# Kernel optimization log

Measured on AMD Instinct MI355X. Metric: run time of the kernel, lower is better.

## Reference

```python
import jax, jax.numpy as jnp
import numpy as np

# Static conv hyperparameters (match init_kwargs / setup_inputs)
PAD = 1
DIL = 1
STRIDE_VAL = 2.5          # continuous stride value used in setup_inputs
INT_STRIDE = 2            # floor(STRIDE_VAL): used for output-size arithmetic (static)


def _bilinear_take(x, pos, axis):
    """Linearly interpolate x along `axis` at fractional positions `pos`.

    pos has shape [O, K]; the sampled axis of x is replaced by the two axes
    (O, K). Out-of-range samples contribute zero (deform-conv convention).
    """
    n = x.shape[axis]
    p0 = jnp.floor(pos).astype(jnp.int32)
    frac = (pos - p0.astype(pos.dtype))
    out_shape = x.shape[:axis] + pos.shape + x.shape[axis + 1:]
    bshape = (1,) * axis + pos.shape + (1,) * (x.ndim - axis - 1)

    def take(p):
        valid = ((p >= 0) & (p < n)).astype(x.dtype).reshape(bshape)
        v = jnp.take(x, jnp.clip(p, 0, n - 1).reshape(-1), axis=axis)
        return v.reshape(out_shape) * valid

    w = frac.reshape(bshape).astype(x.dtype)
    return take(p0) * (1.0 - w) + take(p0 + 1) * w


def setup_inputs() -> dict:
    key = jax.random.key(0)
    k1, k2, k3 = jax.random.split(key, 3)
    x = jax.random.normal(k1, (32, 128, 64, 64), dtype=jnp.float32)
    weight = jax.random.normal(k2, (256, 128, 3, 3), dtype=jnp.float32) * 0.05
    bias = jax.random.normal(k3, (256,), dtype=jnp.float32)
    stride_h = jnp.full((1,), STRIDE_VAL, dtype=jnp.float32)
    stride_w = jnp.full((1,), STRIDE_VAL, dtype=jnp.float32)
    return {"x": x, "weight": weight, "bias": bias,
            "stride_h": stride_h, "stride_w": stride_w}


def reference(x, weight, bias, stride_h, stride_w):
    B, C, H, W = x.shape
    O, _, KH, KW = weight.shape
    # output size uses floor(stride), exactly as StrideConv2dFunction._output_size
    OH = (H + 2 * PAD - DIL * (KH - 1) - 1) // INT_STRIDE + 1
    OW = (W + 2 * PAD - DIL * (KW - 1) - 1) // INT_STRIDE + 1
    # fractional im2col sampling positions: out_idx * stride - pad + k * dilation
    pos_h = (jnp.arange(OH, dtype=jnp.float32)[:, None] * stride_h[0]
             - PAD + jnp.arange(KH, dtype=jnp.float32)[None, :] * DIL)  # [OH,KH]
    pos_w = (jnp.arange(OW, dtype=jnp.float32)[:, None] * stride_w[0]
             - PAD + jnp.arange(KW, dtype=jnp.float32)[None, :] * DIL)  # [OW,KW]
    rows = _bilinear_take(x, pos_h, axis=2)          # [B,C,OH,KH,W]
    patches = _bilinear_take(rows, pos_w, axis=4)    # [B,C,OH,KH,OW,KW]
    out = jnp.einsum('bcpkql,ockl->bopq', patches, weight)  # [B,O,OH,OW]
    return out + bias[None, :, None, None]
```

## Files before the change

### kernel.cpp

```cpp
#include <hip/hip_runtime.h>
#include <cstddef>

#define BB  32
#define CC  128
#define HH  64
#define WW  64
#define OO  256
#define OHH 32
#define OWW 32
#define YSTR 196
#define PSTR 296
#define ROWE (32 * YSTR)

typedef __bf16 bf16x8 __attribute__((ext_vector_type(8)));
typedef __bf16 bf16x4 __attribute__((ext_vector_type(4)));
typedef float  f32x4  __attribute__((ext_vector_type(4)));

__global__ void wtrans_bf16_kernel(const float* __restrict__ w, __bf16* __restrict__ wt) {
    int idx = blockIdx.x * 256 + threadIdx.x;
    if (idx >= OO * 9 * CC) return;
    int c    = idx & 127;
    int rest = idx >> 7;
    int k    = rest % 9;
    int o    = rest / 9;
    wt[idx] = (__bf16)w[((size_t)o * CC + c) * 9 + k];
}

__global__ __launch_bounds__(512, 2)
void conv_mfma_kernel(const float* __restrict__ x, const __bf16* __restrict__ wt,
                      const float* __restrict__ bias, const float* __restrict__ shp,
                      const float* __restrict__ swp, float* __restrict__ out) {
    __shared__ __align__(16) __bf16 yrbuf[4 + 4 * ROWE];
    __shared__ __align__(16) __bf16 pT[128 * PSTR];

    const int tid = threadIdx.x;
    const int b   = blockIdx.x;
    const int p0  = blockIdx.y * 4;
    const float sh = shp[0];
    const float sw = swp[0];

    float fh_[4];
    int   hb_[4];
    bool  oob[4];
#pragma unroll
    for (int pi = 0; pi < 4; ++pi) {
        float hpos = (float)(p0 + pi) * sh - 1.0f;
        float hbf  = floorf(hpos);
        fh_[pi] = hpos - hbf;
        hb_[pi] = (int)hbf;
        oob[pi] = (hb_[pi] >= HH || hb_[pi] <= -4);
    }

    if (oob[0] && oob[1] && oob[2] && oob[3]) {
#pragma unroll
        for (int j = 0; j < 16; ++j) {
            int fi = j * 512 + tid;
            int o  = fi >> 5;
            int rem = fi & 31;
            int pi = rem >> 3;
            int qf = rem & 7;
            float bv = bias[o];
            float4 r; r.x = bv; r.y = bv; r.z = bv; r.w = bv;
            *(float4*)(out + (((size_t)b * OO + o) * OHH + p0 + pi) * OWW + qf * 4) = r;
        }
        return;
    }

    const int piA = tid >> 7;
    const int t7  = tid & 127;
    const int cA  = t7 >> 2;
    const int cg0 = (t7 & 3) * 16;
    const float fhA = fh_[piA];
    int  hrA[4];
    bool rvA[4];
#pragma unroll
    for (int r = 0; r < 4; ++r) {
        hrA[r] = hb_[piA] + r;
        rvA[r] = (hrA[r] >= 0) && (hrA[r] < HH);
    }
    __bf16* yrA = yrbuf + 4 + piA * ROWE;

    const int piB = tid >> 7;
    const int qB  = (tid >> 2) & 31;
    const int cB  = (tid & 3) * 8;
    const float wposB = (float)qB * sw - 1.0f;
    const float wbfB  = floorf(wposB);
    const float fw    = wposB - wbfB;
    const int   wbq   = (int)wbfB;
    const int   wba   = min(wbq & ~3, 60);
    const int   e     = wbq - wba;
    const bool  g1 = e >= 1, g2 = e >= 2, g3 = e >= 3;
    bool mv[4];
#pragma unroll
    for (int j = 0; j < 4; ++j) mv[j] = ((unsigned)(wbq + j) < (unsigned)WW);
    const bool qDead = (wbq >= WW);
    const __bf16* yrB = yrbuf + 4 + piB * ROWE;
    __bf16* pqRow = pT + (piB * 32 + qB) * PSTR;

    const int wv = tid >> 6;
    const int l  = tid & 63;
    const int lr = l & 15;
    const int lg = l >> 4;
    const int o0 = wv * 32;

    f32x4 acc[2][8];
#pragma unroll
    for (int ot = 0; ot < 2; ++ot)
#pragma unroll
        for (int nt = 0; nt < 8; ++nt) acc[ot][nt] = (f32x4)0.0f;

    if (tid < 4) yrbuf[tid] = (__bf16)0.0f;

    if (qDead) {
        bf16x4 z;
        z[0] = (__bf16)0.0f; z[1] = (__bf16)0.0f; z[2] = (__bf16)0.0f; z[3] = (__bf16)0.0f;
#pragma unroll
        for (int kk = 0; kk < 9; ++kk) {
            *(bf16x4*)(pqRow + kk * 32 + cB)     = z;
            *(bf16x4*)(pqRow + kk * 32 + cB + 4) = z;
        }
    }

    for (int chunk = 0; chunk < 4; ++chunk) {
        const int c0 = chunk * 32;

        {
            const float* xp = x + ((size_t)(b * CC + c0 + cA) * HH) * WW;
            float4 v[4][4];
#pragma unroll
            for (int r = 0; r < 4; ++r) {
                if (rvA[r]) {
                    const float* rp = xp + (size_t)hrA[r] * WW + cg0;
#pragma unroll
                    for (int g = 0; g < 4; ++g) v[r][g] = *(const float4*)(rp + g * 4);
                } else {
#pragma unroll
                    for (int g = 0; g < 4; ++g) { v[r][g].x = 0.f; v[r][g].y = 0.f; v[r][g].z = 0.f; v[r][g].w = 0.f; }
                }
            }
            __bf16* yw = yrA + cA * YSTR + cg0;
#pragma unroll
            for (int kh = 0; kh < 3; ++kh) {
#pragma unroll
                for (int g = 0; g < 4; ++g) {
                    bf16x4 t;
                    t[0] = (__bf16)(v[kh][g].x + fhA * (v[kh + 1][g].x - v[kh][g].x));
                    t[1] = (__bf16)(v[kh][g].y + fhA * (v[kh + 1][g].y - v[kh][g].y));
                    t[2] = (__bf16)(v[kh][g].z + fhA * (v[kh + 1][g].z - v[kh][g].z));
                    t[3] = (__bf16)(v[kh][g].w + fhA * (v[kh + 1][g].w - v[kh][g].w));
                    *(bf16x4*)(yw + kh * 64 + g * 4) = t;
                }
            }
        }
        __syncthreads();

        if (!qDead) {
#pragma unroll
            for (int g = 0; g < 2; ++g) {
                const int cc0 = cB + g * 4;
                bf16x4 rlo[12], rhi[12];
#pragma unroll
                for (int ci = 0; ci < 4; ++ci)
#pragma unroll
                    for (int kh = 0; kh < 3; ++kh) {
                        const __bf16* yc = yrB + (cc0 + ci) * YSTR + kh * 64 + wba;
                        rlo[ci * 3 + kh] = *(const bf16x4*)yc;
                        rhi[ci * 3 + kh] = *(const bf16x4*)(yc + 4);
                    }
                float tv[3][3][4];
#pragma unroll
                for (int ci = 0; ci < 4; ++ci)
#pragma unroll
                    for (int kh = 0; kh < 3; ++kh) {
                        bf16x4 a  = rlo[ci * 3 + kh];
                        bf16x4 bq = rhi[ci * 3 + kh];
                        float v0 = (float)a[0], v1 = (float)a[1], v2 = (float)a[2], v3 = (float)a[3];
                        float v4 = (float)bq[0], v5 = (float)bq[1], v6 = (float)bq[2];
                        float s0 = g1 ? v1 : v0; s0 = g2 ? v2 : s0; s0 = g3 ? v3 : s0;
                        float s1 = g1 ? v2 : v1; s1 = g2 ? v3 : s1; s1 = g3 ? v4 : s1;
                        float s2 = g1 ? v3 : v2; s2 = g2 ? v4 : s2; s2 = g3 ? v5 : s2;
                        float s3 = g1 ? v4 : v3; s3 = g2 ? v5 : s3; s3 = g3 ? v6 : s3;
                        s0 = mv[0] ? s0 : 0.0f;
                        s1 = mv[1] ? s1 : 0.0f;
                        s2 = mv[2] ? s2 : 0.0f;
                        s3 = mv[3] ? s3 : 0.0f;
                        tv[kh][0][ci] = s0 + fw * (s1 - s0);
                        tv[kh][1][ci] = s1 + fw * (s2 - s1);
                        tv[kh][2][ci] = s2 + fw * (s3 - s2);
                    }
#pragma unroll
                for (int kh = 0; kh < 3; ++kh)
#pragma unroll
                    for (int kw = 0; kw < 3; ++kw) {
                        bf16x4 pr;
                        pr[0] = (__bf16)tv[kh][kw][0];
                        pr[1] = (__bf16)tv[kh][kw][1];
                        pr[2] = (__bf16)tv[kh][kw][2];
                        pr[3] = (__bf16)tv[kh][kw][3];
                        *(bf16x4*)(pqRow + (kh * 3 + kw) * 32 + cc0) = pr;
                    }
            }
        }
        __syncthreads();

        __builtin_amdgcn_s_setprio(1);
#pragma unroll
        for (int k = 0; k < 9; ++k) {
            const __bf16* wp = wt + ((size_t)(o0 + lr) * 9 + k) * CC + c0 + lg * 8;
            bf16x8 a0 = *(const bf16x8*)(wp);
            bf16x8 a1 = *(const bf16x8*)(wp + (size_t)16 * 9 * CC);
            bf16x8 bfr[8];
#pragma unroll
            for (int nt = 0; nt < 8; ++nt)
                bfr[nt] = *(const bf16x8*)&pT[(nt * 16 + lr) * PSTR + k * 32 + lg * 8];
#pragma unroll
            for (int nt = 0; nt < 8; ++nt) {
                acc[0][nt] = __builtin_amdgcn_mfma_f32_16x16x32_bf16(a0, bfr[nt], acc[0][nt], 0, 0, 0);
                acc[1][nt] = __builtin_amdgcn_mfma_f32_16x16x32_bf16(a1, bfr[nt], acc[1][nt], 0, 0, 0);
            }
        }
        __builtin_amdgcn_s_setprio(0);
    }

#pragma unroll
    for (int ot = 0; ot < 2; ++ot) {
#pragma unroll
        for (int r = 0; r < 4; ++r) {
            int o = o0 + ot * 16 + lg * 4 + r;
            float bv = bias[o];
#pragma unroll
            for (int nt = 0; nt < 8; ++nt) {
                int pi = nt >> 1;
                int qc = (nt & 1) * 16 + lr;
                out[(((size_t)b * OO + o) * OHH + p0 + pi) * OWW + qc] = acc[ot][nt][r] + bv;
            }
        }
    }
}

__global__ __launch_bounds__(256)
void conv_fallback_kernel(const float* __restrict__ x, const float* __restrict__ w,
                          const float* __restrict__ bias, const float* __restrict__ shp,
                          const float* __restrict__ swp, float* __restrict__ out) {
    __shared__ __align__(16) float xr[4][WW];
    __shared__ __align__(16) float patch[9][OWW];
    const int tid = threadIdx.x;
    const int p = blockIdx.y;
    const int b = blockIdx.x;
    const float sh = shp[0];
    const float sw = swp[0];
    const float hpos = (float)p * sh - 1.0f;
    const float hbf  = floorf(hpos);
    const float fh   = hpos - hbf;
    const int   hb   = (int)hbf;
    const int og = tid & 63;
    const int qg = tid >> 6;
    const int o0 = og * 4;
    const int q0 = qg * 8;
    const int rr   = tid >> 6;
    const int colc = tid & 63;
    const int rowg = hb + rr;
    const bool rv = (rowg >= 0) && (rowg < HH);
    float acc[4][8];
#pragma unroll
    for (int i = 0; i < 4; ++i)
#pragma unroll
        for (int j = 0; j < 8; ++j) acc[i][j] = 0.0f;
    for (int c = 0; c < CC; ++c) {
        float vv = 0.0f;
        if (rv) vv = x[(((size_t)b * CC + c) * HH + rowg) * WW + colc];
        xr[rr][colc] = vv;
        __syncthreads();
        for (int it = tid; it < 9 * OWW; it += 256) {
            int k = it >> 5; int q = it & 31;
            int kh = k / 3;  int kw = k - kh * 3;
            float wpos = (float)q * sw - 1.0f + (float)kw;
            float wbf = floorf(wpos);
            float fwl = wpos - wbf;
            int wb = (int)wbf;
            float x00 = 0, x01 = 0, x10 = 0, x11 = 0;
            if (wb >= 0 && wb < WW)         { x00 = xr[kh][wb];     x10 = xr[kh + 1][wb]; }
            if (wb + 1 >= 0 && wb + 1 < WW) { x01 = xr[kh][wb + 1]; x11 = xr[kh + 1][wb + 1]; }
            float top = x00 * (1.0f - fwl) + x01 * fwl;
            float bot = x10 * (1.0f - fwl) + x11 * fwl;
            patch[k][q] = top * (1.0f - fh) + bot * fh;
        }
        __syncthreads();
        const float4* pv = (const float4*)&patch[0][0];
#pragma unroll
        for (int k = 0; k < 9; ++k) {
            const float* wb_ = w + (size_t)o0 * (CC * 9) + c * 9 + k;
            float wvv[4] = {wb_[0], wb_[1 * CC * 9], wb_[2 * CC * 9], wb_[3 * CC * 9]};
            float4 pa = pv[k * 8 + (q0 >> 2)];
            float4 pb = pv[k * 8 + (q0 >> 2) + 1];
#pragma unroll
            for (int oo2 = 0; oo2 < 4; ++oo2) {
                acc[oo2][0] += wvv[oo2] * pa.x; acc[oo2][1] += wvv[oo2] * pa.y;
                acc[oo2][2] += wvv[oo2] * pa.z; acc[oo2][3] += wvv[oo2] * pa.w;
                acc[oo2][4] += wvv[oo2] * pb.x; acc[oo2][5] += wvv[oo2] * pb.y;
                acc[oo2][6] += wvv[oo2] * pb.z; acc[oo2][7] += wvv[oo2] * pb.w;
            }
        }
    }
    float4 bv = ((const float4*)bias)[og];
    float bvv[4] = {bv.x, bv.y, bv.z, bv.w};
#pragma unroll
    for (int oo2 = 0; oo2 < 4; ++oo2) {
        size_t off = (((size_t)b * OO + o0 + oo2) * OHH + p) * OWW + q0;
        float4 r0, r1;
        r0.x = acc[oo2][0] + bvv[oo2]; r0.y = acc[oo2][1] + bvv[oo2];
        r0.z = acc[oo2][2] + bvv[oo2]; r0.w = acc[oo2][3] + bvv[oo2];
        r1.x = acc[oo2][4] + bvv[oo2]; r1.y = acc[oo2][5] + bvv[oo2];
        r1.z = acc[oo2][6] + bvv[oo2]; r1.w = acc[oo2][7] + bvv[oo2];
        *(float4*)(out + off)     = r0;
        *(float4*)(out + off + 4) = r1;
    }
}

extern "C" void kernel_launch(void* const* d_in, const int* in_sizes, int n_in,
                              void* d_out, int out_size, void* d_ws, size_t ws_size,
                              hipStream_t stream) {
    const float* x    = (const float*)d_in[0];
    const float* w    = (const float*)d_in[1];
    const float* bias = (const float*)d_in[2];
    const float* shp  = (const float*)d_in[3];
    const float* swp  = (const float*)d_in[4];
    float* out = (float*)d_out;

    const size_t wt_bytes = (size_t)OO * 9 * CC * sizeof(__bf16);
    if (ws_size >= wt_bytes) {
        __bf16* wtp = (__bf16*)d_ws;
        int n = OO * 9 * CC;
        wtrans_bf16_kernel<<<(n + 255) / 256, 256, 0, stream>>>(w, wtp);
        dim3 grid(BB, OHH / 4);
        conv_mfma_kernel<<<grid, 512, 0, stream>>>(x, wtp, bias, shp, swp, out);
    } else {
        dim3 grid(BB, OHH);
        conv_fallback_kernel<<<grid, 256, 0, stream>>>(x, w, bias, shp, swp, out);
    }
}
```

Baseline: 55.30 us.

## Warp-specialize conv into producer/consumer waves with double-buffered patch tiles

Splits the block into four producer waves and four MFMA consumer waves. The producers do the bilinear row and column interpolation into double-buffered LDS patch slots, and the consumers run the GEMM. They synchronise through workgroup-scope atomic counters with spin-waits instead of block-wide __syncthreads, so patch building for the next channel chunk can overlap the MFMA work on the current one. Each block now covers 2 output rows instead of 4, which doubles the grid and halves LDS use. The cost is that only half the waves issue MFMAs, weight loads are duplicated across twice as many blocks, and spin-wait polling adds overhead.

```diff
diff --git a/kernel.cpp b/kernel.cpp
--- a/kernel.cpp
+++ b/kernel.cpp
@@ -9,8 +9,9 @@
 #define OHH 32
 #define OWW 32
 #define YSTR 196
+#define ROWE (32 * YSTR)
 #define PSTR 296
-#define ROWE (32 * YSTR)
+#define PTSLOT (64 * PSTR)
 
 typedef __bf16 bf16x8 __attribute__((ext_vector_type(8)));
 typedef __bf16 bf16x4 __attribute__((ext_vector_type(4)));
@@ -30,33 +31,34 @@
 void conv_mfma_kernel(const float* __restrict__ x, const __bf16* __restrict__ wt,
                       const float* __restrict__ bias, const float* __restrict__ shp,
                       const float* __restrict__ swp, float* __restrict__ out) {
-    __shared__ __align__(16) __bf16 yrbuf[4 + 4 * ROWE];
-    __shared__ __align__(16) __bf16 pT[128 * PSTR];
+    __shared__ __align__(16) __bf16 yrbuf[4 + 2 * ROWE];
+    __shared__ __align__(16) __bf16 pT[2 * PTSLOT];
+    __shared__ int ydone, pdone, cdone;
 
     const int tid = threadIdx.x;
     const int b   = blockIdx.x;
-    const int p0  = blockIdx.y * 4;
+    const int p0  = blockIdx.y * 2;
     const float sh = shp[0];
     const float sw = swp[0];
 
-    float fh_[4];
-    int   hb_[4];
-    bool  oob[4];
-#pragma unroll
-    for (int pi = 0; pi < 4; ++pi) {
+    float fh_[2];
+    int   hb_[2];
+#pragma unroll
+    for (int pi = 0; pi < 2; ++pi) {
         float hpos = (float)(p0 + pi) * sh - 1.0f;
         float hbf  = floorf(hpos);
         fh_[pi] = hpos - hbf;
         hb_[pi] = (int)hbf;
-        oob[pi] = (hb_[pi] >= HH || hb_[pi] <= -4);
-    }
-
-    if (oob[0] && oob[1] && oob[2] && oob[3]) {
-#pragma unroll
-        for (int j = 0; j < 16; ++j) {
+    }
+    const bool oob0 = (hb_[0] >= HH || hb_[0] <= -4);
+    const bool oob1 = (hb_[1] >= HH || hb_[1] <= -4);
+
+    if (oob0 && oob1) {
+#pragma unroll
+        for (int j = 0; j < 8; ++j) {
             int fi = j * 512 + tid;
-            int o  = fi >> 5;
-            int rem = fi & 31;
+            int o  = fi >> 4;
+            int rem = fi & 15;
             int pi = rem >> 3;
             int qf = rem & 7;
             float bv = bias[o];
@@ -66,173 +68,218 @@
         return;
     }
 
-    const int piA = tid >> 7;
-    const int t7  = tid & 127;
-    const int cA  = t7 >> 2;
-    const int cg0 = (t7 & 3) * 16;
-    const float fhA = fh_[piA];
-    int  hrA[4];
-    bool rvA[4];
-#pragma unroll
-    for (int r = 0; r < 4; ++r) {
-        hrA[r] = hb_[piA] + r;
-        rvA[r] = (hrA[r] >= 0) && (hrA[r] < HH);
-    }
-    __bf16* yrA = yrbuf + 4 + piA * ROWE;
-
-    const int piB = tid >> 7;
-    const int qB  = (tid >> 2) & 31;
-    const int cB  = (tid & 3) * 8;
-    const float wposB = (float)qB * sw - 1.0f;
-    const float wbfB  = floorf(wposB);
-    const float fw    = wposB - wbfB;
-    const int   wbq   = (int)wbfB;
-    const int   wba   = min(wbq & ~3, 60);
-    const int   e     = wbq - wba;
-    const bool  g1 = e >= 1, g2 = e >= 2, g3 = e >= 3;
-    bool mv[4];
-#pragma unroll
-    for (int j = 0; j < 4; ++j) mv[j] = ((unsigned)(wbq + j) < (unsigned)WW);
-    const bool qDead = (wbq >= WW);
-    const __bf16* yrB = yrbuf + 4 + piB * ROWE;
-    __bf16* pqRow = pT + (piB * 32 + qB) * PSTR;
+    if (tid == 0) { ydone = 0; pdone = 0; cdone = 0; }
+    if (tid < 4) yrbuf[tid] = (__bf16)0.0f;
+    __syncthreads();
 
     const int wv = tid >> 6;
     const int l  = tid & 63;
     const int lr = l & 15;
     const int lg = l >> 4;
-    const int o0 = wv * 32;
-
-    f32x4 acc[2][8];
-#pragma unroll
-    for (int ot = 0; ot < 2; ++ot)
-#pragma unroll
-        for (int nt = 0; nt < 8; ++nt) acc[ot][nt] = (f32x4)0.0f;
-
-    if (tid < 4) yrbuf[tid] = (__bf16)0.0f;
-
-    if (qDead) {
-        bf16x4 z;
-        z[0] = (__bf16)0.0f; z[1] = (__bf16)0.0f; z[2] = (__bf16)0.0f; z[3] = (__bf16)0.0f;
-#pragma unroll
-        for (int kk = 0; kk < 9; ++kk) {
-            *(bf16x4*)(pqRow + kk * 32 + cB)     = z;
-            *(bf16x4*)(pqRow + kk * 32 + cB + 4) = z;
-        }
-    }
-
-    for (int chunk = 0; chunk < 4; ++chunk) {
-        const int c0 = chunk * 32;
-
-        {
-            const float* xp = x + ((size_t)(b * CC + c0 + cA) * HH) * WW;
-            float4 v[4][4];
-#pragma unroll
-            for (int r = 0; r < 4; ++r) {
-                if (rvA[r]) {
-                    const float* rp = xp + (size_t)hrA[r] * WW + cg0;
-#pragma unroll
-                    for (int g = 0; g < 4; ++g) v[r][g] = *(const float4*)(rp + g * 4);
-                } else {
-#pragma unroll
-                    for (int g = 0; g < 4; ++g) { v[r][g].x = 0.f; v[r][g].y = 0.f; v[r][g].z = 0.f; v[r][g].w = 0.f; }
+
+    auto waitge = [&](int* f, int t) {
+        while (__hip_atomic_load(f, __ATOMIC_RELAXED, __HIP_MEMORY_SCOPE_WORKGROUP) < t)
+            __builtin_amdgcn_s_sleep(2);
+        __threadfence_block();
+        __builtin_amdgcn_sched_barrier(0);
+    };
+    auto post = [&](int* f) {
+        __threadfence_block();
+        if ((tid & 63) == 0)
+            __hip_atomic_fetch_add(f, 1, __ATOMIC_RELAXED, __HIP_MEMORY_SCOPE_WORKGROUP);
+    };
+
+    if (wv < 4) {
+        const int piA = tid >> 7;
+        const int t7  = tid & 127;
+        const int cA  = t7 >> 2;
+        const int cg0 = (t7 & 3) * 16;
+        const float fhA = fh_[piA];
+        int  hrA[4];
+        bool rvA[4];
+#pragma unroll
+        for (int r = 0; r < 4; ++r) {
+            hrA[r] = hb_[piA] + r;
+            rvA[r] = (hrA[r] >= 0) && (hrA[r] < HH);
+        }
+        __bf16* yrA = yrbuf + 4 + piA * ROWE;
+
+        const int qB2  = tid >> 2;
+        const int pi2B = qB2 >> 5;
+        const int qB   = qB2 & 31;
+        const int cB   = (tid & 3) * 8;
+        const float wposB = (float)qB * sw - 1.0f;
+        const float wbfB  = floorf(wposB);
+        const float fw    = wposB - wbfB;
+        const int   wbq   = (int)wbfB;
+        const int   wba   = min(wbq & ~3, 60);
+        const int   e     = wbq - wba;
+        const bool  g1 = e >= 1, g2 = e >= 2, g3 = e >= 3;
+        bool mv[4];
+#pragma unroll
+        for (int j = 0; j < 4; ++j) mv[j] = ((unsigned)(wbq + j) < (unsigned)WW);
+        const bool qDead = (wbq >= WW);
+        const __bf16* yrB = yrbuf + 4 + pi2B * ROWE;
+
+        if (qDead) {
+            bf16x4 z;
+            z[0] = (__bf16)0.0f; z[1] = (__bf16)0.0f; z[2] = (__bf16)0.0f; z[3] = (__bf16)0.0f;
+#pragma unroll
+            for (int s = 0; s < 2; ++s) {
+                __bf16* pq = pT + s * PTSLOT + qB2 * PSTR;
+#pragma unroll
+                for (int kk = 0; kk < 9; ++kk) {
+                    *(bf16x4*)(pq + kk * 32 + cB)     = z;
+                    *(bf16x4*)(pq + kk * 32 + cB + 4) = z;
                 }
             }
-            __bf16* yw = yrA + cA * YSTR + cg0;
-#pragma unroll
-            for (int kh = 0; kh < 3; ++kh) {
-#pragma unroll
-                for (int g = 0; g < 4; ++g) {
-                    bf16x4 t;
-                    t[0] = (__bf16)(v[kh][g].x + fhA * (v[kh + 1][g].x - v[kh][g].x));
-                    t[1] = (__bf16)(v[kh][g].y + fhA * (v[kh + 1][g].y - v[kh][g].y));
-                    t[2] = (__bf16)(v[kh][g].z + fhA * (v[kh + 1][g].z - v[kh][g].z));
-                    t[3] = (__bf16)(v[kh][g].w + fhA * (v[kh + 1][g].w - v[kh][g].w));
-                    *(bf16x4*)(yw + kh * 64 + g * 4) = t;
+        }
+
+        for (int c = 0; c < 4; ++c) {
+            const int c0 = c * 32;
+            if (c >= 1) waitge(&pdone, 4 * c);
+
+            {
+                const float* xp = x + ((size_t)(b * CC + c0 + cA) * HH) * WW;
+                float4 v[4][4];
+#pragma unroll
+                for (int r = 0; r < 4; ++r) {
+                    if (rvA[r]) {
+                        const float* rp = xp + (size_t)hrA[r] * WW + cg0;
+#pragma unroll
+                        for (int g = 0; g < 4; ++g) v[r][g] = *(const float4*)(rp + g * 4);
+                    } else {
+#pragma unroll
+                        for (int g = 0; g < 4; ++g) { v[r][g].x = 0.f; v[r][g].y = 0.f; v[r][g].z = 0.f; v[r][g].w = 0.f; }
+                    }
                 }
-            }
-        }
-        __syncthreads();
-
-        if (!qDead) {
-#pragma unroll
-            for (int g = 0; g < 2; ++g) {
-                const int cc0 = cB + g * 4;
-                bf16x4 rlo[12], rhi[12];
-#pragma unroll
-                for (int ci = 0; ci < 4; ++ci)
-#pragma unroll
-                    for (int kh = 0; kh < 3; ++kh) {
-                        const __bf16* yc = yrB + (cc0 + ci) * YSTR + kh * 64 + wba;
-                        rlo[ci * 3 + kh] = *(const bf16x4*)yc;
-                        rhi[ci * 3 + kh] = *(const bf16x4*)(yc + 4);
+                __bf16* yw = yrA + cA * YSTR + cg0;
+#pragma unroll
+                for (int kh = 0; kh < 3; ++kh)
+#pragma unroll
+                    for (int g = 0; g < 4; ++g) {
+                        bf16x4 t;
+                        t[0] = (__bf16)(v[kh][g].x + fhA * (v[kh + 1][g].x - v[kh][g].x));
+                        t[1] = (__bf16)(v[kh][g].y + fhA * (v[kh + 1][g].y - v[kh][g].y));
+                        t[2] = (__bf16)(v[kh][g].z + fhA * (v[kh + 1][g].z - v[kh][g].z));
+                        t[3] = (__bf16)(v[kh][g].w + fhA * (v[kh + 1][g].w - v[kh][g].w));
+                        *(bf16x4*)(yw + kh * 64 + g * 4) = t;
                     }
-                float tv[3][3][4];
-#pragma unroll
-                for (int ci = 0; ci < 4; ++ci)
-#pragma unroll
-                    for (int kh = 0; kh < 3; ++kh) {
-                        bf16x4 a  = rlo[ci * 3 + kh];
-                        bf16x4 bq = rhi[ci * 3 + kh];
-                        float v0 = (float)a[0], v1 = (float)a[1], v2 = (float)a[2], v3 = (float)a[3];
-                        float v4 = (float)bq[0], v5 = (float)bq[1], v6 = (float)bq[2];
-                        float s0 = g1 ? v1 : v0; s0 = g2 ? v2 : s0; s0 = g3 ? v3 : s0;
-                        float s1 = g1 ? v2 : v1; s1 = g2 ? v3 : s1; s1 = g3 ? v4 : s1;
-                        float s2 = g1 ? v3 : v2; s2 = g2 ? v4 : s2; s2 = g3 ? v5 : s2;
-                        float s3 = g1 ? v4 : v3; s3 = g2 ? v5 : s3; s3 = g3 ? v6 : s3;
-                        s0 = mv[0] ? s0 : 0.0f;
-                        s1 = mv[1] ? s1 : 0.0f;
-                        s2 = mv[2] ? s2 : 0.0f;
-                        s3 = mv[3] ? s3 : 0.0f;
-                        tv[kh][0][ci] = s0 + fw * (s1 - s0);
-                        tv[kh][1][ci] = s1 + fw * (s2 - s1);
-                        tv[kh][2][ci] = s2 + fw * (s3 - s2);
-                    }
-#pragma unroll
-                for (int kh = 0; kh < 3; ++kh)
-#pragma unroll
-                    for (int kw = 0; kw < 3; ++kw) {
-                        bf16x4 pr;
-                        pr[0] = (__bf16)tv[kh][kw][0];
-                        pr[1] = (__bf16)tv[kh][kw][1];
-                        pr[2] = (__bf16)tv[kh][kw][2];
-                        pr[3] = (__bf16)tv[kh][kw][3];
-                        *(bf16x4*)(pqRow + (kh * 3 + kw) * 32 + cc0) = pr;
-                    }
-            }
-        }
-        __syncthreads();
-
+            }
+            post(&ydone);
+            waitge(&ydone, 4 * (c + 1));
+            if (c >= 2) waitge(&cdone, 4 * (c - 1));
+
+            if (!qDead) {
+                __bf16* pqRow = pT + (c & 1) * PTSLOT + qB2 * PSTR;
+#pragma unroll
+                for (int g = 0; g < 2; ++g) {
+                    const int cc0 = cB + g * 4;
+                    bf16x4 rlo[12], rhi[12];
+#pragma unroll
+                    for (int ci = 0; ci < 4; ++ci)
+#pragma unroll
+                        for (int kh = 0; kh < 3; ++kh) {
+                            const __bf16* yc = yrB + (cc0 + ci) * YSTR + kh * 64 + wba;
+                            rlo[ci * 3 + kh] = *(const bf16x4*)yc;
+                            rhi[ci * 3 + kh] = *(const bf16x4*)(yc + 4);
+                        }
+                    float tv[3][3][4];
+#pragma unroll
+                    for (int ci = 0; ci < 4; ++ci)
+#pragma unroll
+                        for (int kh = 0; kh < 3; ++kh) {
+                            bf16x4 a  = rlo[ci * 3 + kh];
+                            bf16x4 bq = rhi[ci * 3 + kh];
+                            float v0 = (float)a[0], v1 = (float)a[1], v2 = (float)a[2], v3 = (float)a[3];
+                            float v4 = (float)bq[0], v5 = (float)bq[1], v6 = (float)bq[2];
+                            float s0 = g1 ? v1 : v0; s0 = g2 ? v2 : s0; s0 = g3 ? v3 : s0;
+                            float s1 = g1 ? v2 : v1; s1 = g2 ? v3 : s1; s1 = g3 ? v4 : s1;
+                            float s2 = g1 ? v3 : v2; s2 = g2 ? v4 : s2; s2 = g3 ? v5 : s2;
+                            float s3 = g1 ? v4 : v3; s3 = g2 ? v5 : s3; s3 = g3 ? v6 : s3;
+                            s0 = mv[0] ? s0 : 0.0f;
+                            s1 = mv[1] ? s1 : 0.0f;
+                            s2 = mv[2] ? s2 : 0.0f;
+                            s3 = mv[3] ? s3 : 0.0f;
+                            tv[kh][0][ci] = s0 + fw * (s1 - s0);
+                            tv[kh][1][ci] = s1 + fw * (s2 - s1);
+                            tv[kh][2][ci] = s2 + fw * (s3 - s2);
+                        }
+#pragma unroll
+                    for (int kh = 0; kh < 3; ++kh)
+#pragma unroll
+                        for (int kw = 0; kw < 3; ++kw) {
+                            bf16x4 pr;
+                            pr[0] = (__bf16)tv[kh][kw][0];
+                            pr[1] = (__bf16)tv[kh][kw][1];
+                            pr[2] = (__bf16)tv[kh][kw][2];
+                            pr[3] = (__bf16)tv[kh][kw][3];
+                            *(bf16x4*)(pqRow + (kh * 3 + kw) * 32 + cc0) = pr;
+                        }
+                }
+            }
+            post(&pdone);
+        }
+        return;
+    }
+
+    const int o0 = (wv - 4) * 64;
+    f32x4 acc[4][4];
+#pragma unroll
+    for (int ot = 0; ot < 4; ++ot)
+#pragma unroll
+        for (int nt = 0; nt < 4; ++nt) acc[ot][nt] = (f32x4)0.0f;
+
+#pragma unroll
+    for (int c = 0; c < 4; ++c) {
+        const int c0 = c * 32;
+        waitge(&pdone, 4 * (c + 1));
+        const __bf16* pTs = pT + (c & 1) * PTSLOT;
         __builtin_amdgcn_s_setprio(1);
 #pragma unroll
         for (int k = 0; k < 9; ++k) {
             const __bf16* wp = wt + ((size_t)(o0 + lr) * 9 + k) * CC + c0 + lg * 8;
             bf16x8 a0 = *(const bf16x8*)(wp);
             bf16x8 a1 = *(const bf16x8*)(wp + (size_t)16 * 9 * CC);
-            bf16x8 bfr[8];
-#pragma unroll
-            for (int nt = 0; nt < 8; ++nt)
-                bfr[nt] = *(const bf16x8*)&pT[(nt * 16 + lr) * PSTR + k * 32 + lg * 8];
-#pragma unroll
-            for (int nt = 0; nt < 8; ++nt) {
-                acc[0][nt] = __builtin_amdgcn_mfma_f32_16x16x32_bf16(a0, bfr[nt], acc[0][nt], 0, 0, 0);
-                acc[1][nt] = __builtin_amdgcn_mfma_f32_16x16x32_bf16(a1, bfr[nt], acc[1][nt], 0, 0, 0);
-            }
+            bf16x8 a2 = *(const bf16x8*)(wp + (size_t)32 * 9 * CC);
+            bf16x8 a3 = *(const bf16x8*)(wp + (size_t)48 * 9 * CC);
+            bf16x8 b0 = *(const bf16x8*)&pTs[(0  + lr) * PSTR + k * 32 + lg * 8];
+            bf16x8 b1 = *(const bf16x8*)&pTs[(16 + lr) * PSTR + k * 32 + lg * 8];
+            bf16x8 b2 = *(const bf16x8*)&pTs[(32 + lr) * PSTR + k * 32 + lg * 8];
+            bf16x8 b3 = *(const bf16x8*)&pTs[(48 + lr) * PSTR + k * 32 + lg * 8];
+            acc[0][0] = __builtin_amdgcn_mfma_f32_16x16x32_bf16(a0, b0, acc[0][0], 0, 0, 0);
+            acc[0][1] = __builtin_amdgcn_mfma_f32_16x16x32_bf16(a0, b1, acc[0][1], 0, 0, 0);
+            acc[0][2] = __builtin_amdgcn_mfma_f32_16x16x32_bf16(a0, b2, acc[0][2], 0, 0, 0);
+            acc[0][3] = __builtin_amdgcn_mfma_f32_16x16x32_bf16(a0, b3, acc[0][3], 0, 0, 0);
+            acc[1][0] = __builtin_amdgcn_mfma_f32_16x16x32_bf16(a1, b0, acc[1][0], 0, 0, 0);
+            acc[1][1] = __builtin_amdgcn_mfma_f32_16x16x32_bf16(a1, b1, acc[1][1], 0, 0, 0);
+            acc[1][2] = __builtin_amdgcn_mfma_f32_16x16x32_bf16(a1, b2, acc[1][2], 0, 0, 0);
+            acc[1][3] = __builtin_amdgcn_mfma_f32_16x16x32_bf16(a1, b3, acc[1][3], 0, 0, 0);
+            acc[2][0] = __builtin_amdgcn_mfma_f32_16x16x32_bf16(a2, b0, acc[2][0], 0, 0, 0);
+            acc[2][1] = __builtin_amdgcn_mfma_f32_16x16x32_bf16(a2, b1, acc[2][1], 0, 0, 0);
+            acc[2][2] = __builtin_amdgcn_mfma_f32_16x16x32_bf16(a2, b2, acc[2][2], 0, 0, 0);
+            acc[2][3] = __builtin_amdgcn_mfma_f32_16x16x32_bf16(a2, b3, acc[2][3], 0, 0, 0);
+            acc[3][0] = __builtin_amdgcn_mfma_f32_16x16x32_bf16(a3, b0, acc[3][0], 0, 0, 0);
+            acc[3][1] = __builtin_amdgcn_mfma_f32_16x16x32_bf16(a3, b1, acc[3][1], 0, 0, 0);
+            acc[3][2] = __builtin_amdgcn_mfma_f32_16x16x32_bf16(a3, b2, acc[3][2], 0, 0, 0);
+            acc[3][3] = __builtin_amdgcn_mfma_f32_16x16x32_bf16(a3, b3, acc[3][3], 0, 0, 0);
         }
         __builtin_amdgcn_s_setprio(0);
-    }
-
-#pragma unroll
-    for (int ot = 0; ot < 2; ++ot) {
+        post(&cdone);
+    }
+
+#pragma unroll
+    for (int ot = 0; ot < 4; ++ot) {
 #pragma unroll
         for (int r = 0; r < 4; ++r) {
             int o = o0 + ot * 16 + lg * 4 + r;
             float bv = bias[o];
 #pragma unroll
-            for (int nt = 0; nt < 8; ++nt) {
-                int pi = nt >> 1;
-                int qc = (nt & 1) * 16 + lr;
-                out[(((size_t)b * OO + o) * OHH + p0 + pi) * OWW + qc] = acc[ot][nt][r] + bv;
+            for (int nt = 0; nt < 4; ++nt) {
+                int n  = nt * 16 + lr;
+                int pi = n >> 5;
+                int q  = n & 31;
+                out[(((size_t)b * OO + o) * OHH + p0 + pi) * OWW + q] = acc[ot][nt][r] + bv;
             }
         }
     }
@@ -332,7 +379,7 @@
         __bf16* wtp = (__bf16*)d_ws;
         int n = OO * 9 * CC;
         wtrans_bf16_kernel<<<(n + 255) / 256, 256, 0, stream>>>(w, wtp);
-        dim3 grid(BB, OHH / 4);
+        dim3 grid(BB, OHH / 2);
         conv_mfma_kernel<<<grid, 512, 0, stream>>>(x, wtp, bias, shp, swp, out);
     } else {
         dim3 grid(BB, OHH);
```

Result: slower. 69.88 us (+26.4%).
